# Kernel tuning notes

Hardware: AMD Instinct MI355X
Metric: run time of the kernel (lower is better)

## Reference

```python
import jax, jax.numpy as jnp
import numpy as np
from jax import lax

B, T, L, OUT, SP, E, H = 128, 300, 28, 28, 7, 20, 256
W = T - L + 1          # 273 sliding windows
W_OUT = W - OUT        # 245 training windows
F_IN = L + 1 + E       # 49 rnn input features


def _lstm_dilated(x, d, Wih, Whh, b):
    # x: [T0, B, F]; dilation d realized by phase-stacking time into batch (zalando DRNN scheme)
    T0, Bn, F = x.shape
    pad = (-T0) % d
    if pad:
        x = jnp.concatenate([x, jnp.zeros((pad, Bn, F), x.dtype)], axis=0)
    Tn = x.shape[0] // d
    xd = x.reshape(Tn, d * Bn, F)  # element [k, j*Bn:(j+1)*Bn] == x[k*d+j]
    Hh = Whh.shape[1]

    def step(carry, xt):
        h, c = carry
        z = xt @ Wih.T + h @ Whh.T + b
        i, f, g, o = jnp.split(z, 4, axis=-1)  # torch LSTM gate order i,f,g,o
        c = jax.nn.sigmoid(f) * c + jax.nn.sigmoid(i) * jnp.tanh(g)
        h = jax.nn.sigmoid(o) * jnp.tanh(c)
        return (h, c), h

    h0 = jnp.zeros((d * Bn, Hh), x.dtype)
    _, hs = lax.scan(step, (h0, h0), xd)
    return hs.reshape(Tn * d, Bn, Hh)[:T0]


def _forward(train_dataset, val_dataset, alpha_raw, gamma_raw, init_seas,
             input_categories, my_param,
             Wih1, Whh1, b1, Wih2, Whh2, b2, Wih3, Whh3, b3, Wih4, Whh4, b4,
             linear_W, linear_b, score_W, score_b):
    x = train_dataset
    a = jax.nn.sigmoid(alpha_raw)   # [B]
    g = jax.nn.sigmoid(gamma_raw)   # [B]
    S0 = jnp.exp(init_seas)         # [B,7] = seasonalities[0..6]
    s7 = S0[:, 0]                   # seasonalities[7] = exp(init[:,0])
    level0 = x[:, 0] / S0[:, 0]
    buf0 = jnp.concatenate([S0[:, 1:], s7[:, None]], axis=1)  # S[1..7], shift register

    def es_step(carry, xt):
        level, buf = carry
        s = buf[:, 0]
        lvl = a * (xt / s) + (1.0 - a) * level
        s_new = g * (xt / lvl) + (1.0 - g) * s
        buf = jnp.concatenate([buf[:, 1:], s_new[:, None]], axis=1)
        return (lvl, buf), (lvl, s_new)

    _, (lvls, s_news) = lax.scan(es_step, (level0, buf0), x[:, 1:].T)
    levels = jnp.concatenate([level0[None], lvls], axis=0).T        # [B,T]
    S_full = jnp.concatenate([S0, s7[:, None], s_news.T], axis=1)   # [B,T+7]
    # extension: cat(S_full, S_full[:, T : T-7+28])  -> [B, T+28]
    S_ext = jnp.concatenate([S_full, S_full[:, T:T - SP + OUT]], axis=1)

    # input windows (vectorized over all W window positions)
    widx = jnp.arange(W)[:, None] + jnp.arange(L)[None, :]          # [W,L]
    lvl_w = levels[:, L - 1 + jnp.arange(W)]                        # [B,W]
    norm_in = x[:, widx] / S_ext[:, widx] / lvl_w[:, :, None]       # [B,W,L]
    cats = jnp.broadcast_to(input_categories[:, None, :], (B, W, E))
    cat_in = jnp.concatenate([norm_in, cats], axis=2)[jnp.arange(B) % 10]  # original j%10 row pick
    mp = jnp.broadcast_to(my_param.reshape(1, 1, 1), (B, W, 1))
    window_input = jnp.transpose(jnp.concatenate([cat_in, mp], axis=2), (1, 0, 2))  # [W,B,F_IN]

    # output windows
    oidx = (L + jnp.arange(W_OUT))[:, None] + jnp.arange(OUT)[None, :]  # [W_OUT,OUT]
    lvl_o = levels[:, L - 1 + jnp.arange(W_OUT)]                        # [B,W_OUT]
    window_output = jnp.transpose(x[:, oidx] / S_ext[:, oidx] / lvl_o[:, :, None], (1, 0, 2))

    # residual dilated LSTM stack: block1 dilations (1,2); block2 dilations (2,6) + residual
    h1 = _lstm_dilated(window_input, 1, Wih1, Whh1, b1)
    h1 = _lstm_dilated(h1, 2, Wih2, Whh2, b2)
    h2 = _lstm_dilated(h1, 2, Wih3, Whh3, b3)
    h2 = _lstm_dilated(h2, 6, Wih4, Whh4, b4) + h1
    h = jnp.tanh(h2 @ linear_W.T + linear_b)
    rnn_out = h @ score_W.T + score_b                                   # [W,B,OUT]

    # LSTM stack is causal, so running on window_input[:-OUT] equals slicing the full run
    prediction_values = rnn_out[:-OUT]
    actual_values = window_output
    holdout = rnn_out[-1] * S_ext[:, -OUT:] * levels[:, -1:]
    holdout_prediction = holdout * (holdout > 0).astype(holdout.dtype)
    hav = val_dataset
    hav_norm = hav / S_ext[:, -OUT:] / levels[:, -1:]
    return (prediction_values, actual_values, holdout_prediction, rnn_out, hav, hav_norm)


def setup_inputs() -> dict:
    key = jax.random.key(0)
    ks = jax.random.split(key, 24)
    s = float(1.0 / np.sqrt(H))
    u = lambda k, shape: jax.random.uniform(k, shape, jnp.float32, -s, s)
    inp = {
        "train_dataset": jax.random.uniform(ks[0], (B, T), jnp.float32) * 2.0 + 0.5,  # positive sales
        "val_dataset": jax.random.uniform(ks[1], (B, OUT), jnp.float32) * 2.0 + 0.5,
        "alpha_raw": jnp.full((B,), 0.5, jnp.float32),
        "gamma_raw": jnp.full((B,), 0.5, jnp.float32),
        "init_seas": jnp.full((B, SP), 0.5, jnp.float32),
        "input_categories": jnp.full((B, E), 0.001, jnp.float32) + 0.01 * jax.random.normal(ks[2], (B, E), jnp.float32),
        "my_param": jnp.full((1,), 0.001, jnp.float32),
        "Wih1": u(ks[3], (4 * H, F_IN)), "Whh1": u(ks[4], (4 * H, H)), "b1": u(ks[5], (4 * H,)),
        "Wih2": u(ks[6], (4 * H, H)), "Whh2": u(ks[7], (4 * H, H)), "b2": u(ks[8], (4 * H,)),
        "Wih3": u(ks[9], (4 * H, H)), "Whh3": u(ks[10], (4 * H, H)), "b3": u(ks[11], (4 * H,)),
        "Wih4": u(ks[12], (4 * H, H)), "Whh4": u(ks[13], (4 * H, H)), "b4": u(ks[14], (4 * H,)),
        "linear_W": u(ks[15], (H, H)), "linear_b": u(ks[16], (H,)),
        "score_W": u(ks[17], (OUT, H)), "score_b": u(ks[18], (OUT,)),
    }
    return inp


def reference(train_dataset, val_dataset, alpha_raw, gamma_raw, init_seas,
              input_categories, my_param,
              Wih1, Whh1, b1, Wih2, Whh2, b2, Wih3, Whh3, b3, Wih4, Whh4, b4,
              linear_W, linear_b, score_W, score_b):
    return _forward(train_dataset, val_dataset, alpha_raw, gamma_raw, init_seas,
                    input_categories, my_param,
                    Wih1, Whh1, b1, Wih2, Whh2, b2, Wih3, Whh3, b3, Wih4, Whh4, b4,
                    linear_W, linear_b, score_W, score_b)
```

## Files before the change

kernel.cpp:

```cpp
#include <hip/hip_runtime.h>

typedef unsigned short u16;
typedef unsigned int   u32;

static __device__ __forceinline__ float sigf (float x){ return 1.0f/(1.0f+__expf(-x)); }
static __device__ __forceinline__ float tanh_(float x){ return 2.0f/(1.0f+__expf(-2.0f*x)) - 1.0f; }

#define NM 2730
#define N_O0 878080
#define N_O3 978432

static __device__ __forceinline__ int dot4(u32 a, u32 b, int acc){
#if __has_builtin(__builtin_amdgcn_sdot4)
  return __builtin_amdgcn_sdot4((int)a, (int)b, acc, false);
#else
  int s = acc;
  #pragma unroll
  for(int i=0;i<4;i++){
    int av = (int)((signed char)((a >> (8*i)) & 0xffu));
    int bv = (int)((signed char)((b >> (8*i)) & 0xffu));
    s += av*bv;
  }
  return s;
#endif
}

__global__ __launch_bounds__(256) void k_prep(
    const float* __restrict__ x,     float* __restrict__ xT,
    const float* __restrict__ wi0,   float* __restrict__ wT0,
    const float* __restrict__ wi1,   float* __restrict__ wT1,
    const float* __restrict__ wi2,   float* __restrict__ wT2,
    const float* __restrict__ wi3,   float* __restrict__ wT3,
    const float* __restrict__ lw,    float* __restrict__ lwT,
    const float* __restrict__ sw,    float* __restrict__ swT,
    const float* __restrict__ h0, const float* __restrict__ h1,
    const float* __restrict__ h2, const float* __restrict__ h3,
    float* __restrict__ zsc){
  int i = blockIdx.x*256 + threadIdx.x;
  if(i < 38400){
    int t = i >> 7, b = i & 127;
    xT[i] = x[b*300 + t];
    return;
  }
  i -= 38400;
  if(i < 50176){ int c=i/1024, r=i-c*1024; wT0[i] = wi0[r*49 + c];  return; }
  i -= 50176;
  if(i < 262144){ int c=i>>10, r=i&1023; wT1[i] = wi1[r*256 + c];   return; }
  i -= 262144;
  if(i < 262144){ int c=i>>10, r=i&1023; wT2[i] = wi2[r*256 + c];   return; }
  i -= 262144;
  if(i < 262144){ int c=i>>10, r=i&1023; wT3[i] = wi3[r*256 + c];   return; }
  i -= 262144;
  if(i < 65536){ int c=i>>8, r=i&255; lwT[i] = lw[r*256 + c];       return; }
  i -= 65536;
  if(i < 7168){ int c=i/28, r=i-c*28; swT[i] = sw[r*256 + c];       return; }
  i -= 7168;
  if(i < 4096){
    int l = i >> 10, r = i & 1023;
    const float* W = (l==0)?h0:(l==1)?h1:(l==2)?h2:h3;
    const float4* p = (const float4*)(W + (size_t)r*256);
    float m = 0.f;
    #pragma unroll 8
    for(int q=0;q<64;q++){
      float4 v = p[q];
      m = fmaxf(m, fmaxf(fmaxf(fabsf(v.x),fabsf(v.y)), fmaxf(fabsf(v.z),fabsf(v.w))));
    }
    zsc[i] = fmaxf(m, 1e-20f) * (1.0f/16129.0f);
  }
}

__global__ __launch_bounds__(256) void k_packes(
    const float* __restrict__ h0, const float* __restrict__ h1,
    const float* __restrict__ h2, const float* __restrict__ h3,
    const float* __restrict__ zsc, u32* __restrict__ W8,
    const float* __restrict__ xT, const float* __restrict__ alpha,
    const float* __restrict__ gamma, const float* __restrict__ iseas,
    float* __restrict__ ST, float* __restrict__ lvlT){
  if(blockIdx.x < 1024){
    int i = blockIdx.x*256 + threadIdx.x;
    int l = i >> 16;
    int uidx = i & 65535;
    int dw = uidx & 3;
    int kg = (uidx >> 2) & 127;
    int q  = (uidx >> 9) & 3;
    int rr = (uidx >> 11) & 7;
    int js = uidx >> 14;
    int row = rr*128 + kg;
    int k0  = js*64 + q*16 + dw*4;
    const float* W = (l==0)?h0:(l==1)?h1:(l==2)?h2:h3;
    float inv = 1.0f / (zsc[l*1024 + row] * 127.0f);
    u32 out = 0;
    #pragma unroll
    for(int b=0;b<4;b++){
      float v = W[(size_t)row*256 + k0 + b];
      int q8 = max(-127, min(127, __float2int_rn(v * inv)));
      out |= ((u32)(q8 & 0xff)) << (8*b);
    }
    W8[i] = out;
    return;
  }
  int b = threadIdx.x;
  if(b >= 128) return;
  float a = sigf(alpha[b]);
  float g = sigf(gamma[b]);
  float S0[7];
  #pragma unroll
  for(int i=0;i<7;i++){ S0[i] = __expf(iseas[b*7+i]); ST[i*128+b] = S0[i]; }
  ST[7*128+b] = S0[0];
  float q0=S0[1],q1=S0[2],q2=S0[3],q3=S0[4],q4=S0[5],q5=S0[6],q6=S0[0];
  float lvl = xT[b]/S0[0];
  lvlT[b] = lvl;
  for(int t=1;t<300;t++){
    float xt = xT[t*128+b];
    float s  = q0;
    lvl = a*(xt/s) + (1.0f-a)*lvl;
    float sn = g*(xt/lvl) + (1.0f-g)*s;
    q0=q1;q1=q2;q2=q3;q3=q4;q4=q5;q5=q6;q6=sn;
    lvlT[t*128+b]   = lvl;
    ST[(t+7)*128+b] = sn;
  }
}

__global__ __launch_bounds__(256) void k_gemm1(
    const float* __restrict__ xT, const float* __restrict__ ST,
    const float* __restrict__ lvlT, const float* __restrict__ cats,
    const float* __restrict__ mp,
    const float* __restrict__ WT,
    const float* __restrict__ bias,
    float* __restrict__ Z){
  __shared__ float Xs[8][52];
  const int tid = threadIdx.x;
  const int m0 = blockIdx.x*8;
  for(int idx=tid; idx<8*49; idx+=256){
    int p = idx/49, f = idx - p*49;
    int m = m0+p;
    float v = 0.f;
    if(m < NM){
      int tt = m/10, jj = m - (m/10)*10;
      if(f < 28){
        int c = tt + f;
        v = xT[c*128 + jj] / ST[c*128 + jj] / lvlT[(tt+27)*128 + jj];
      } else if(f < 48){
        v = cats[jj*20 + (f-28)];
      } else {
        v = mp[0];
      }
    }
    Xs[p][f] = v;
  }
  __syncthreads();
  float acc0[8], acc1[8], acc2[8], acc3[8];
  {
    float b0 = bias[tid];
    float b1 = bias[tid+256];
    float b2 = bias[tid+512];
    float b3 = bias[tid+768];
    #pragma unroll
    for(int p=0;p<8;p++){ acc0[p]=b0; acc1[p]=b1; acc2[p]=b2; acc3[p]=b3; }
  }
  #pragma unroll 7
  for(int f=0; f<49; f++){
    float w0 = WT[f*1024 + tid      ];
    float w1 = WT[f*1024 + tid+256  ];
    float w2 = WT[f*1024 + tid+512  ];
    float w3 = WT[f*1024 + tid+768  ];
    #pragma unroll
    for(int p=0;p<8;p++){
      float xv = Xs[p][f];
      acc0[p] += w0*xv; acc1[p] += w1*xv; acc2[p] += w2*xv; acc3[p] += w3*xv;
    }
  }
  for(int p=0;p<8;p++){
    int m = m0+p;
    if(m < NM){
      float* zb = Z + m*1024 + tid;
      zb[0]=acc0[p]; zb[256]=acc1[p]; zb[512]=acc2[p]; zb[768]=acc3[p];
    }
  }
}

__global__ __launch_bounds__(256) void k_gemm(const float* __restrict__ X,
                                              const float* __restrict__ WT,
                                              const float* __restrict__ bias,
                                              float* __restrict__ Z){
  __shared__ float Xs[8][256];
  const int tid = threadIdx.x;
  const int m0 = blockIdx.x*8;
  for(int p=0;p<8;p++){
    int m = m0+p;
    Xs[p][tid] = (m < NM) ? X[m*256+tid] : 0.0f;
  }
  __syncthreads();
  float acc0[8], acc1[8], acc2[8], acc3[8];
  {
    float b0 = bias[tid];
    float b1 = bias[tid+256];
    float b2 = bias[tid+512];
    float b3 = bias[tid+768];
    #pragma unroll
    for(int p=0;p<8;p++){ acc0[p]=b0; acc1[p]=b1; acc2[p]=b2; acc3[p]=b3; }
  }
  #pragma unroll 4
  for(int f=0; f<256; f++){
    float w0 = WT[f*1024 + tid      ];
    float w1 = WT[f*1024 + tid+256  ];
    float w2 = WT[f*1024 + tid+512  ];
    float w3 = WT[f*1024 + tid+768  ];
    #pragma unroll
    for(int p=0;p<8;p++){
      float xv = Xs[p][f];
      acc0[p] += w0*xv; acc1[p] += w1*xv; acc2[p] += w2*xv; acc3[p] += w3*xv;
    }
  }
  for(int p=0;p<8;p++){
    int m = m0+p;
    if(m < NM){
      float* zb = Z + m*1024 + tid;
      zb[0]=acc0[p]; zb[256]=acc1[p]; zb[512]=acc2[p]; zb[768]=acc3[p];
    }
  }
}

__global__ __launch_bounds__(512) void k_scan8(
    const float* __restrict__ Z,
    const u32* __restrict__ W8,
    const float* __restrict__ zsc,
    float* __restrict__ Y,
    const float* __restrict__ RES,
    int d){
  __shared__ __align__(16) u32 h8[64];
  __shared__ int   zp[4][1024];
  __shared__ float sc[1024];
  __shared__ __align__(16) u32 wl[5*2048];
  const int tid = threadIdx.x;
  const int chain = blockIdx.x;
  const int j = chain % 10;
  const int r = chain / 10;
  const int ns = (273 - r + d - 1)/d;
  const int kg = tid & 127;
  const int js = tid >> 7;
  const uint4* Wb = (const uint4*)W8 + (size_t)js*4096 + kg;
  const uint4* hq = (const uint4*)h8 + js*4;
  uint4* wl4 = (uint4*)wl;

  for(int i=tid;i<1024;i+=512) sc[i] = zsc[i];
  #pragma unroll
  for(int rr=0;rr<5;rr++) wl4[rr*512 + tid] = Wb[rr*512];
  if(tid < 64) h8[tid] = 0u;
  float cst = 0.0f;
  __syncthreads();

  int t = r;
  for(int s=0; s<ns; s++, t+=d){
    const size_t row = (size_t)(t*10 + j);
    float zv0=0.f, zv1=0.f, zv2=0.f, zv3=0.f, rv=0.f;
    if(tid < 256){
      const float* zb = Z + row*1024;
      zv0 = zb[tid]; zv1 = zb[tid+256]; zv2 = zb[tid+512]; zv3 = zb[tid+768];
      if(RES) rv = RES[row*256 + tid];
    }
    int a0=0,a1=0,a2=0,a3=0,a4=0,a5=0,a6=0,a7=0;
    #pragma unroll
    for(int q=0;q<4;q++){
      uint4 h4 = hq[q];
      #pragma unroll
      for(int rr=0;rr<8;rr++){
        uint4 w = (q==0 && rr<5) ? wl4[rr*512 + tid] : Wb[rr*512 + q*128];
        int* ap = (rr==0)?&a0:(rr==1)?&a1:(rr==2)?&a2:(rr==3)?&a3:
                  (rr==4)?&a4:(rr==5)?&a5:(rr==6)?&a6:&a7;
        int acc = *ap;
        acc = dot4(w.x, h4.x, acc);
        acc = dot4(w.y, h4.y, acc);
        acc = dot4(w.z, h4.z, acc);
        acc = dot4(w.w, h4.w, acc);
        *ap = acc;
      }
    }
    zp[js][       kg] = a0;
    zp[js][128  + kg] = a1;
    zp[js][256  + kg] = a2;
    zp[js][384  + kg] = a3;
    zp[js][512  + kg] = a4;
    zp[js][640  + kg] = a5;
    zp[js][768  + kg] = a6;
    zp[js][896  + kg] = a7;
    __syncthreads();
    if(tid < 256){
      const int u = tid;
      int si = zp[0][u]     + zp[1][u]     + zp[2][u]     + zp[3][u];
      int sf = zp[0][u+256] + zp[1][u+256] + zp[2][u+256] + zp[3][u+256];
      int sg = zp[0][u+512] + zp[1][u+512] + zp[2][u+512] + zp[3][u+512];
      int so = zp[0][u+768] + zp[1][u+768] + zp[2][u+768] + zp[3][u+768];
      float zi = zv0 + sc[u]     * (float)si;
      float zf = zv1 + sc[u+256] * (float)sf;
      float zg = zv2 + sc[u+512] * (float)sg;
      float zo = zv3 + sc[u+768] * (float)so;
      float c  = sigf(zf)*cst + sigf(zi)*tanh_(zg);
      float h  = sigf(zo)*tanh_(c);
      cst = c;
      int hqi = __float2int_rn(h * 127.0f);
      hqi = max(-127, min(127, hqi));
      ((signed char*)h8)[u] = (signed char)hqi;
      Y[row*256 + u] = h + rv;
    }
    __syncthreads();
  }
}

__global__ __launch_bounds__(256) void k_headout(const float* __restrict__ Y4,
    const float* __restrict__ LWT,
    const float* __restrict__ lb,
    const float* __restrict__ SWT,
    const float* __restrict__ sb,
    const float* __restrict__ ST, const float* __restrict__ lvlT,
    const float* __restrict__ xT, const float* __restrict__ val,
    float* __restrict__ out){
  __shared__ float v [8][256];
  __shared__ float h2[8][256];
  const int tid = threadIdx.x;
  if(blockIdx.x >= 342){
    int i = (blockIdx.x - 342)*256 + tid;
    if(i < N_O0){
      int o = i % 28;
      int b = (i/28) % 128;
      int t = i/(28*128);
      int c = 28 + t + o;
      out[878080 + i] = xT[c*128+b] / ST[c*128+b] / lvlT[(27+t)*128+b];
    } else {
      i -= N_O0;
      if(i < 3584){
        int b = i/28, o = i%28;
        int col = (o < 21) ? (286+o) : (279+o);
        float Sm = ST[col*128 + b];
        float lv = lvlT[299*128 + b];
        out[2738176 + i] = val[i];
        out[2741760 + i] = val[i] / Sm / lv;
      }
    }
    return;
  }
  const int m0 = blockIdx.x*8;
  for(int p=0;p<8;p++){
    int m = m0+p;
    v[p][tid] = (m<NM) ? Y4[m*256+tid] : 0.0f;
  }
  __syncthreads();
  float acc[8];
  float bz = lb[tid];
  #pragma unroll
  for(int p=0;p<8;p++) acc[p]=bz;
  #pragma unroll 4
  for(int f=0; f<256; f++){
    float w = LWT[f*256+tid];
    #pragma unroll
    for(int p=0;p<8;p++) acc[p] += w * v[p][f];
  }
  #pragma unroll
  for(int p=0;p<8;p++) h2[p][tid] = tanh_(acc[p]);
  __syncthreads();
  if(tid < 224){
    int o = tid % 28, p = tid / 28;
    int m = m0 + p;
    if(m < NM){
      float a = sb[o];
      for(int f=0; f<256; f++) a += SWT[f*28+o] * h2[p][f];
      int t = m / 10, j = m - t*10;
      float* o0 = out;
      float* o3 = out + 1759744;
      for(int b=j; b<128; b+=10){
        size_t idx = (size_t)t*3584 + b*28 + o;
        o3[idx] = a;
        if(t < 245) o0[idx] = a;
      }
      if(t == 272){
        int col = (o < 21) ? (286+o) : (279+o);
        float* o2 = out + 1756160;
        for(int b=j; b<128; b+=10){
          float hv = a * ST[col*128 + b] * lvlT[299*128 + b];
          o2[b*28 + o] = (hv > 0.0f) ? hv : 0.0f;
        }
      }
    }
  }
}

extern "C" void kernel_launch(void* const* d_in, const int* in_sizes, int n_in,
                              void* d_out, int out_size, void* d_ws, size_t ws_size,
                              hipStream_t stream){
  (void)in_sizes; (void)n_in; (void)out_size; (void)ws_size;
  const float* x     = (const float*)d_in[0];
  const float* val   = (const float*)d_in[1];
  const float* alpha = (const float*)d_in[2];
  const float* gamma = (const float*)d_in[3];
  const float* iseas = (const float*)d_in[4];
  const float* cats  = (const float*)d_in[5];
  const float* mp    = (const float*)d_in[6];
  const float* Wih[4]  = {(const float*)d_in[7],  (const float*)d_in[10], (const float*)d_in[13], (const float*)d_in[16]};
  const float* Whh[4]  = {(const float*)d_in[8],  (const float*)d_in[11], (const float*)d_in[14], (const float*)d_in[17]};
  const float* bias[4] = {(const float*)d_in[9],  (const float*)d_in[12], (const float*)d_in[15], (const float*)d_in[18]};
  const float* linW  = (const float*)d_in[19];
  const float* linb  = (const float*)d_in[20];
  const float* scW   = (const float*)d_in[21];
  const float* scb   = (const float*)d_in[22];

  float* Fw   = (float*)d_ws;
  float* ST   = Fw;
  float* lvlT = ST   + 39296;
  float* xT   = lvlT + 38400;
  float* xz   = xT   + 38400;
  float* yA   = xz   + 2795520;
  float* yB   = yA   + 698880;
  float* wihT[4];
  wihT[0] = yB + 698880;
  wihT[1] = wihT[0] + 50176;
  wihT[2] = wihT[1] + 262144;
  wihT[3] = wihT[2] + 262144;
  float* linWT = wihT[3] + 262144;
  float* scT   = linWT + 65536;
  float* zsc   = scT   + 7168;
  u32*   W8all = (u32*)(zsc + 4096);

  k_prep<<<3718, 256, 0, stream>>>(x, xT,
      Wih[0], wihT[0], Wih[1], wihT[1], Wih[2], wihT[2], Wih[3], wihT[3],
      linW, linWT, scW, scT,
      Whh[0], Whh[1], Whh[2], Whh[3], zsc);

  k_packes<<<1025, 256, 0, stream>>>(Whh[0], Whh[1], Whh[2], Whh[3], zsc, W8all,
                                     xT, alpha, gamma, iseas, ST, lvlT);

  const int    dlt[4]    = {1, 2, 2, 6};
  const int    chains[4] = {10, 20, 20, 60};
  const float* Xin[4]    = {nullptr, yA, yB, yA};
  float*       Yout[4]   = {yA, yB, yA, yA};
  for(int l=0;l<4;l++){
    if(l == 0)
      k_gemm1<<<(NM+7)/8, 256, 0, stream>>>(xT, ST, lvlT, cats, mp,
                                            wihT[0], bias[0], xz);
    else
      k_gemm<<<(NM+7)/8, 256, 0, stream>>>(Xin[l], wihT[l], bias[l], xz);
    k_scan8<<<chains[l], 512, 0, stream>>>(xz, W8all + l*65536, zsc + l*1024,
                                           Yout[l],
                                           (l==3) ? yB : (const float*)nullptr, dlt[l]);
  }

  k_headout<<<342 + (N_O0 + 3584 + 255)/256, 256, 0, stream>>>(
      yA, linWT, linb, scT, scb, ST, lvlT, xT, val, (float*)d_out);
}
```

Baseline: 1.037 ms.

## Split head/output kernel, coalesce output writes, stage ES input in LDS

The fused head/output kernel becomes two kernels. k_head writes compact per-window scores to a workspace buffer, and k_outs writes all outputs with coalesced stores, using LDS to transpose the normalized-input block. The ES recurrence now reads its input series from a transposed shared-memory copy instead of strided global loads. The scan kernel stops caching part of the int8 weights in LDS, which cuts shared memory and may raise occupancy but reloads those weights from cache every step. It also swaps __syncthreads for an explicit lgkmcnt wait plus barrier. The extra launch and intermediate buffer add some overhead.

```diff
diff --git a/kernel.cpp b/kernel.cpp
--- a/kernel.cpp
+++ b/kernel.cpp
@@ -1,14 +1,12 @@
 #include <hip/hip_runtime.h>
 
-typedef unsigned short u16;
-typedef unsigned int   u32;
+typedef unsigned int u32;
 
 static __device__ __forceinline__ float sigf (float x){ return 1.0f/(1.0f+__expf(-x)); }
 static __device__ __forceinline__ float tanh_(float x){ return 2.0f/(1.0f+__expf(-2.0f*x)) - 1.0f; }
 
 #define NM 2730
 #define N_O0 878080
-#define N_O3 978432
 
 static __device__ __forceinline__ int dot4(u32 a, u32 b, int acc){
 #if __has_builtin(__builtin_amdgcn_sdot4)
@@ -76,6 +74,7 @@
     const float* __restrict__ xT, const float* __restrict__ alpha,
     const float* __restrict__ gamma, const float* __restrict__ iseas,
     float* __restrict__ ST, float* __restrict__ lvlT){
+  __shared__ float xs[128*301];
   if(blockIdx.x < 1024){
     int i = blockIdx.x*256 + threadIdx.x;
     int l = i >> 16;
@@ -99,6 +98,11 @@
     W8[i] = out;
     return;
   }
+  for(int i=threadIdx.x; i<38400; i+=256){
+    int t = i >> 7, b = i & 127;
+    xs[b*301 + t] = xT[i];
+  }
+  __syncthreads();
   int b = threadIdx.x;
   if(b >= 128) return;
   float a = sigf(alpha[b]);
@@ -108,10 +112,10 @@
   for(int i=0;i<7;i++){ S0[i] = __expf(iseas[b*7+i]); ST[i*128+b] = S0[i]; }
   ST[7*128+b] = S0[0];
   float q0=S0[1],q1=S0[2],q2=S0[3],q3=S0[4],q4=S0[5],q5=S0[6],q6=S0[0];
-  float lvl = xT[b]/S0[0];
+  float lvl = xs[b*301]/S0[0];
   lvlT[b] = lvl;
   for(int t=1;t<300;t++){
-    float xt = xT[t*128+b];
+    float xt = xs[b*301 + t];
     float s  = q0;
     lvl = a*(xt/s) + (1.0f-a)*lvl;
     float sn = g*(xt/lvl) + (1.0f-g)*s;
@@ -231,7 +235,6 @@
   __shared__ __align__(16) u32 h8[64];
   __shared__ int   zp[4][1024];
   __shared__ float sc[1024];
-  __shared__ __align__(16) u32 wl[5*2048];
   const int tid = threadIdx.x;
   const int chain = blockIdx.x;
   const int j = chain % 10;
@@ -241,11 +244,8 @@
   const int js = tid >> 7;
   const uint4* Wb = (const uint4*)W8 + (size_t)js*4096 + kg;
   const uint4* hq = (const uint4*)h8 + js*4;
-  uint4* wl4 = (uint4*)wl;
 
   for(int i=tid;i<1024;i+=512) sc[i] = zsc[i];
-  #pragma unroll
-  for(int rr=0;rr<5;rr++) wl4[rr*512 + tid] = Wb[rr*512];
   if(tid < 64) h8[tid] = 0u;
   float cst = 0.0f;
   __syncthreads();
@@ -265,7 +265,7 @@
       uint4 h4 = hq[q];
       #pragma unroll
       for(int rr=0;rr<8;rr++){
-        uint4 w = (q==0 && rr<5) ? wl4[rr*512 + tid] : Wb[rr*512 + q*128];
+        uint4 w = Wb[rr*512 + q*128];
         int* ap = (rr==0)?&a0:(rr==1)?&a1:(rr==2)?&a2:(rr==3)?&a3:
                   (rr==4)?&a4:(rr==5)?&a5:(rr==6)?&a6:&a7;
         int acc = *ap;
@@ -303,42 +303,19 @@
       ((signed char*)h8)[u] = (signed char)hqi;
       Y[row*256 + u] = h + rv;
     }
-    __syncthreads();
-  }
-}
-
-__global__ __launch_bounds__(256) void k_headout(const float* __restrict__ Y4,
+    asm volatile("s_waitcnt lgkmcnt(0)\n\ts_barrier" ::: "memory");
+  }
+}
+
+__global__ __launch_bounds__(256) void k_head(const float* __restrict__ Y4,
     const float* __restrict__ LWT,
     const float* __restrict__ lb,
     const float* __restrict__ SWT,
     const float* __restrict__ sb,
-    const float* __restrict__ ST, const float* __restrict__ lvlT,
-    const float* __restrict__ xT, const float* __restrict__ val,
-    float* __restrict__ out){
+    float* __restrict__ rnnS){
   __shared__ float v [8][256];
   __shared__ float h2[8][256];
   const int tid = threadIdx.x;
-  if(blockIdx.x >= 342){
-    int i = (blockIdx.x - 342)*256 + tid;
-    if(i < N_O0){
-      int o = i % 28;
-      int b = (i/28) % 128;
-      int t = i/(28*128);
-      int c = 28 + t + o;
-      out[878080 + i] = xT[c*128+b] / ST[c*128+b] / lvlT[(27+t)*128+b];
-    } else {
-      i -= N_O0;
-      if(i < 3584){
-        int b = i/28, o = i%28;
-        int col = (o < 21) ? (286+o) : (279+o);
-        float Sm = ST[col*128 + b];
-        float lv = lvlT[299*128 + b];
-        out[2738176 + i] = val[i];
-        out[2741760 + i] = val[i] / Sm / lv;
-      }
-    }
-    return;
-  }
   const int m0 = blockIdx.x*8;
   for(int p=0;p<8;p++){
     int m = m0+p;
@@ -364,21 +341,58 @@
     if(m < NM){
       float a = sb[o];
       for(int f=0; f<256; f++) a += SWT[f*28+o] * h2[p][f];
-      int t = m / 10, j = m - t*10;
-      float* o0 = out;
-      float* o3 = out + 1759744;
-      for(int b=j; b<128; b+=10){
-        size_t idx = (size_t)t*3584 + b*28 + o;
-        o3[idx] = a;
-        if(t < 245) o0[idx] = a;
-      }
-      if(t == 272){
+      rnnS[m*28 + o] = a;
+    }
+  }
+}
+
+__global__ __launch_bounds__(256) void k_outs(
+    const float* __restrict__ rnnS, const float* __restrict__ ST,
+    const float* __restrict__ lvlT, const float* __restrict__ xT,
+    const float* __restrict__ val,  float* __restrict__ out,
+    int nblk){
+  const int tid = threadIdx.x;
+  const int bid = blockIdx.x;
+  if(bid < 245){
+    __shared__ float av[28*132];
+    const int t = bid;
+    for(int i=tid; i<28*128; i+=256){
+      int o = i >> 7, b = i & 127;
+      int c = 28 + t + o;
+      av[o*132 + b] = xT[c*128+b] / ST[c*128+b] / lvlT[(27+t)*128+b];
+    }
+    __syncthreads();
+    for(int i=tid; i<3584; i+=256){
+      int b = i/28, o = i - b*28;
+      out[878080 + t*3584 + i] = av[o*132 + b];
+    }
+    return;
+  }
+  const int stride = (nblk - 245)*256;
+  for(int i0 = (bid-245)*256 + tid; i0 < 978432 + 3584 + 3584; i0 += stride){
+    int i = i0;
+    if(i < 978432){
+      int t = i/3584; int rr = i - t*3584;
+      int b = rr/28;  int o = rr - b*28;
+      int j = b % 10;
+      float a = rnnS[(t*10 + j)*28 + o];
+      out[1759744 + i] = a;
+      if(t < 245) out[i] = a;
+    } else { i -= 978432;
+      if(i < 3584){
+        int b = i/28, o = i - (i/28)*28;
+        int j = b % 10;
+        float a = rnnS[(2720 + j)*28 + o];
         int col = (o < 21) ? (286+o) : (279+o);
-        float* o2 = out + 1756160;
-        for(int b=j; b<128; b+=10){
-          float hv = a * ST[col*128 + b] * lvlT[299*128 + b];
-          o2[b*28 + o] = (hv > 0.0f) ? hv : 0.0f;
-        }
+        float hv = a * ST[col*128 + b] * lvlT[299*128 + b];
+        out[1756160 + i] = (hv > 0.0f) ? hv : 0.0f;
+      } else { i -= 3584;
+        int b = i/28, o = i - (i/28)*28;
+        int col = (o < 21) ? (286+o) : (279+o);
+        float Sm = ST[col*128 + b];
+        float lv = lvlT[299*128 + b];
+        out[2738176 + i] = val[i];
+        out[2741760 + i] = val[i] / Sm / lv;
       }
     }
   }
@@ -419,6 +433,7 @@
   float* scT   = linWT + 65536;
   float* zsc   = scT   + 7168;
   u32*   W8all = (u32*)(zsc + 4096);
+  float* rnnS  = (float*)(W8all + 262144);
 
   k_prep<<<3718, 256, 0, stream>>>(x, xT,
       Wih[0], wihT[0], Wih[1], wihT[1], Wih[2], wihT[2], Wih[3], wihT[3],
@@ -443,6 +458,7 @@
                                            (l==3) ? yB : (const float*)nullptr, dlt[l]);
   }
 
-  k_headout<<<342 + (N_O0 + 3584 + 255)/256, 256, 0, stream>>>(
-      yA, linWT, linb, scT, scb, ST, lvlT, xT, val, (float*)d_out);
-}
+  k_head<<<(NM+7)/8, 256, 0, stream>>>(yA, linWT, linb, scT, scb, rnnS);
+  const int nblk = 245 + 1024;
+  k_outs<<<nblk, 256, 0, stream>>>(rnnS, ST, lvlT, xT, val, (float*)d_out, nblk);
+}
```

Result: faster. 958.6 us (-7.5%).
